# Optimization experiments

Hardware: AMD Instinct MI355X
Metric: run time of the kernel (lower is better)

The kernel has to match this reference:

```python
import jax, jax.numpy as jnp
import numpy as np
from itertools import product

B = 2
X, Y, Z = 96, 96, 192          # voxel grid (x, y, t)
NPB = 300_000                   # occupied voxels per batch item
PX, PY, PZ = X // 2, Y // 2, Z // 4  # pooled grid (kernel/stride [2,2,4])
CIN, COUT, KVOL, NCONV = 32, 64, 27, 2
EPS = 1e-5


def _build_maps():
    """Builds sparse coordinates, maxpool segment ids and 3x3x3 conv kernel maps
    (gather/scatter index pairs per kernel offset), mirroring MinkowskiEngine's
    coordinate manager."""
    rng = np.random.default_rng(0)
    coords = []
    for b in range(B):
        lin = rng.choice(X * Y * Z, NPB, replace=False)
        x = lin // (Y * Z)
        y = (lin // Z) % Y
        z = lin % Z
        coords.append(np.stack([np.full(NPB, b), x, y, z], 1))
    c = np.concatenate(coords).astype(np.int64)  # [N,4] (b,x,y,z)
    # max-pool coord map: out coord = (x//2, y//2, z//4)
    pk = ((c[:, 0] * PX + c[:, 1] // 2) * PY + c[:, 2] // 2) * PZ + c[:, 3] // 4
    uniq, inv = np.unique(pk, return_inverse=True)
    M = len(uniq)
    pz = uniq % PZ
    py = (uniq // PZ) % PY
    px = (uniq // (PZ * PY)) % PX
    pb = uniq // (PZ * PY * PX)
    lut = np.full(B * PX * PY * PZ, -1, np.int64)
    lut[uniq] = np.arange(M)
    ins, outs = [], []
    for dx, dy, dz in product((-1, 0, 1), repeat=3):
        nx, ny, nz = px + dx, py + dy, pz + dz
        ok = (nx >= 0) & (nx < PX) & (ny >= 0) & (ny < PY) & (nz >= 0) & (nz < PZ)
        nk = ((pb * PX + np.clip(nx, 0, PX - 1)) * PY + np.clip(ny, 0, PY - 1)) * PZ + np.clip(nz, 0, PZ - 1)
        j = np.where(ok, lut[nk], -1)
        sel = j >= 0
        ins.append(j[sel])
        outs.append(np.arange(M)[sel])
    L = max(len(a) for a in ins)
    ci = np.full((KVOL, L), M, np.int64)  # pad -> index M (zero row)
    co = np.full((KVOL, L), M, np.int64)  # pad -> dummy out row M (dropped)
    for k in range(KVOL):
        ci[k, : len(ins[k])] = ins[k]
        co[k, : len(outs[k])] = outs[k]
    return inv.astype(np.int64), ci, co, M


def setup_inputs() -> dict:
    key = jax.random.key(0)
    ks = jax.random.split(key, 4)
    pool_seg, ci, co, M = _build_maps()
    N = B * NPB
    feats = jax.random.normal(ks[0], (N, CIN), jnp.float32)
    Wd = jax.random.normal(ks[1], (CIN, COUT), jnp.float32) / np.sqrt(CIN)
    W1 = jax.random.normal(ks[2], (KVOL, COUT, COUT), jnp.float32) / np.sqrt(KVOL * COUT)
    W2 = jax.random.normal(ks[3], (KVOL, COUT, COUT), jnp.float32) / np.sqrt(KVOL * COUT)
    ones = jnp.ones((COUT,), jnp.float32)
    zeros = jnp.zeros((COUT,), jnp.float32)
    return {
        "feats": feats, "Wd": Wd,
        "g0": ones, "b0": zeros,
        "W1": W1, "g1": ones, "b1": zeros,
        "W2": W2, "g2": ones, "b2": zeros,
        "pool_seg": jnp.asarray(pool_seg),
        "conv_in": jnp.asarray(ci), "conv_out": jnp.asarray(co),
        "num_pooled": int(M),
    }


def _bn(h, g, b):
    # training-mode batch norm over all sparse points (biased variance, eps=1e-5)
    m = h.mean(0)
    v = jnp.mean((h - m) ** 2, 0)
    return (h - m) * (g / jnp.sqrt(v + EPS)) + b


def _sparse_conv(h, W, conv_in, conv_out, M):
    # gather-GEMM-scatter over 27 kernel offsets (MinkowskiConvolution, bias=False)
    C = W.shape[-1]
    hp = jnp.concatenate([h, jnp.zeros((1, h.shape[1]), h.dtype)])  # zero pad row
    out = jnp.zeros((M + 1, C), h.dtype)
    for k in range(W.shape[0]):
        out = out.at[conv_out[k]].add(hp[conv_in[k]] @ W[k])
    return out[:M]


def reference(feats, Wd, g0, b0, W1, g1, b1, W2, g2, b2,
              pool_seg, conv_in, conv_out, num_pooled):
    # down_conv (1x1, bias=False) -> BN -> ELU
    h = jax.nn.elu(_bn(feats @ Wd, g0, b0))
    # MinkowskiMaxPooling kernel=stride=[2,2,4] == segment max over pooled cells
    down = jax.ops.segment_max(h, pool_seg, num_segments=num_pooled)
    # nConvs LUConv blocks: ELU(BN(conv3x3x3(x)))
    o = down
    for W, g, b in ((W1, g1, b1), (W2, g2, b2)):
        o = jax.nn.elu(_bn(_sparse_conv(o, W, conv_in, conv_out, num_pooled), g, b))
    # residual add + ELU
    return jax.nn.elu(o + down)
```

## Files before the change

### kernel.cpp

```cpp
#include <hip/hip_runtime.h>
#include <math.h>

#define CIN  32
#define COUT 64
#define KVOL 27
#define EPSF 1e-5f

typedef __attribute__((ext_vector_type(8))) short          short8;
typedef __attribute__((ext_vector_type(8))) unsigned short u16x8;
typedef __attribute__((ext_vector_type(4))) float          float4v;

__device__ __forceinline__ float eluf(float x) { return x > 0.f ? x : expm1f(x); }

__device__ __forceinline__ unsigned short f2bf(float x) {
    unsigned u = __float_as_uint(x);
    unsigned r = (u + 0x7FFFu + ((u >> 16) & 1u)) >> 16;
    return (unsigned short)r;
}
__device__ __forceinline__ unsigned pk2bf(float lo, float hi) {
    return (unsigned)f2bf(lo) | ((unsigned)f2bf(hi) << 16);
}
__device__ __forceinline__ float bf2f(unsigned short h) {
    return __uint_as_float(((unsigned)h) << 16);
}

__global__ void cvt_w_kernel(const float* __restrict__ W1, const float* __restrict__ W2,
                             const float* __restrict__ Wd,
                             unsigned short* __restrict__ Wt1, unsigned short* __restrict__ Wt2,
                             unsigned short* __restrict__ Wdt)
{
    int b = blockIdx.x;
    int t = threadIdx.x;
    if (b == 54) {
        for (int e = t; e < CIN * COUT; e += 256) {
            int i = e >> 6, c = e & 63;
            Wdt[c * CIN + i] = f2bf(Wd[e]);
        }
        return;
    }
    const float* W = (b < 27) ? W1 : W2;
    unsigned short* Wt = (b < 27) ? Wt1 : Wt2;
    int k = (b < 27) ? b : b - 27;
    const float* src = W + (size_t)k * (COUT * COUT);
    unsigned short* dst = Wt + (size_t)k * (COUT * COUT);
    for (int e = t; e < COUT * COUT; e += 256) {
        int i = e >> 6, c = e & 63;
        dst[c * COUT + i] = f2bf(src[e]);
    }
}

__global__ __launch_bounds__(256) void gemm_t_kernel(
    const float* __restrict__ feats, const unsigned short* __restrict__ Wdt,
    int N, unsigned short* __restrict__ t_bf, float* __restrict__ red0)
{
    __shared__ float red_s[64];
    __shared__ float red_q[64];
    int t = threadIdx.x;
    if (t < 64) { red_s[t] = 0.f; red_q[t] = 0.f; }
    __syncthreads();

    int w = t >> 6, lane = t & 63, l15 = lane & 15, quad = lane >> 4;

    short8 aw[4];
    #pragma unroll
    for (int mt = 0; mt < 4; ++mt)
        aw[mt] = *(const short8*)(Wdt + (size_t)(16 * mt + l15) * CIN + quad * 8);

    float s1[16], sq[16];
    #pragma unroll
    for (int e = 0; e < 16; ++e) { s1[e] = 0.f; sq[e] = 0.f; }

    int numTiles = (N + 15) >> 4;
    int stride = gridDim.x * 4;
    int tile = blockIdx.x * 4 + w;

    float4 c0 = make_float4(0.f, 0.f, 0.f, 0.f), c1 = c0;
    {
        int pt = tile * 16 + l15;
        if (tile < numTiles && pt < N) {
            const float4* s = (const float4*)(feats + (size_t)pt * CIN + quad * 8);
            c0 = s[0]; c1 = s[1];
        }
    }

    while (tile < numTiles) {
        int nt = tile + stride;
        float4 n0 = make_float4(0.f, 0.f, 0.f, 0.f), n1 = n0;
        {
            int npt = nt * 16 + l15;
            if (nt < numTiles && npt < N) {
                const float4* s = (const float4*)(feats + (size_t)npt * CIN + quad * 8);
                n0 = s[0]; n1 = s[1];
            }
        }
        union { short8 v; unsigned u[4]; } b;
        b.u[0] = pk2bf(c0.x, c0.y);
        b.u[1] = pk2bf(c0.z, c0.w);
        b.u[2] = pk2bf(c1.x, c1.y);
        b.u[3] = pk2bf(c1.z, c1.w);

        float4v acc[4];
        #pragma unroll
        for (int mt = 0; mt < 4; ++mt)
            acc[mt] = __builtin_amdgcn_mfma_f32_16x16x32_bf16(
                aw[mt], b.v, (float4v){0.f, 0.f, 0.f, 0.f}, 0, 0, 0);

        int pt = tile * 16 + l15;
        if (pt < N) {
            #pragma unroll
            for (int mt = 0; mt < 4; ++mt) {
                uint2 o;
                o.x = pk2bf(acc[mt][0], acc[mt][1]);
                o.y = pk2bf(acc[mt][2], acc[mt][3]);
                *(uint2*)(t_bf + (size_t)pt * COUT + mt * 16 + quad * 4) = o;
            }
        }
        #pragma unroll
        for (int mt = 0; mt < 4; ++mt)
            #pragma unroll
            for (int e = 0; e < 4; ++e) {
                float v = acc[mt][e];
                s1[mt * 4 + e] += v; sq[mt * 4 + e] += v * v;
            }
        c0 = n0; c1 = n1;
        tile = nt;
    }

    #pragma unroll
    for (int m = 1; m <= 8; m <<= 1) {
        #pragma unroll
        for (int e = 0; e < 16; ++e) {
            s1[e] += __shfl_xor(s1[e], m);
            sq[e] += __shfl_xor(sq[e], m);
        }
    }
    if (l15 == 0) {
        #pragma unroll
        for (int e = 0; e < 16; ++e) {
            int ch = (e >> 2) * 16 + quad * 4 + (e & 3);
            atomicAdd(&red_s[ch], s1[e]);
            atomicAdd(&red_q[ch], sq[e]);
        }
    }
    __syncthreads();
    float* dst = red0 + (size_t)(blockIdx.x & 3) * 128;
    if (t < 64)       atomicAdd(&dst[t], red_s[t]);
    else if (t < 128) atomicAdd(&dst[t], red_q[t - 64]);
}

__global__ void fin0_kernel(const float* __restrict__ red, const float* __restrict__ g,
                            const float* __restrict__ b, float* __restrict__ scale,
                            float* __restrict__ shift, int cnt)
{
    int c = threadIdx.x;
    float s = 0.f, q = 0.f;
    #pragma unroll
    for (int i = 0; i < 4; ++i) { s += red[i * 128 + c]; q += red[i * 128 + 64 + c]; }
    float m = s / (float)cnt;
    float var = q / (float)cnt - m * m;
    float sc = g[c] / sqrtf(var + EPSF);
    scale[c] = sc;
    shift[c] = b[c] - m * sc;
}

__global__ void bucket_kernel(const int* __restrict__ pool_seg,
                              int* __restrict__ cnt, int* __restrict__ bucket, int N)
{
    int j = blockIdx.x * 256 + threadIdx.x;
    if (j < N) {
        int s = pool_seg[j];
        int pos = atomicAdd(&cnt[s], 1);
        bucket[(size_t)s * 16 + pos] = j;
    }
}

__global__ __launch_bounds__(256) void pool_max_kernel(
    const unsigned short* __restrict__ t_bf,
    const int* __restrict__ cnt, const int* __restrict__ bucket,
    const float* __restrict__ scale0, const float* __restrict__ shift0,
    unsigned short* __restrict__ down_bf, int M)
{
    int id = blockIdx.x * 256 + threadIdx.x;
    int s = id >> 4, cg = id & 15;
    if (s >= M) return;
    int n = cnt[s];
    const int4* bk4 = (const int4*)(bucket + (size_t)s * 16);
    float4 mx = make_float4(-INFINITY, -INFINITY, -INFINITY, -INFINITY);
    float4 mn = make_float4( INFINITY,  INFINITY,  INFINITY,  INFINITY);
    #pragma unroll
    for (int ch = 0; ch < 4; ++ch) {
        if (ch * 4 >= n) break;
        int4 b4 = bk4[ch];
        #pragma unroll
        for (int e = 0; e < 4; ++e) {
            int p = ch * 4 + e;
            if (p < n) {
                int idx = (e == 0) ? b4.x : (e == 1) ? b4.y : (e == 2) ? b4.z : b4.w;
                ushort4 v = *(const ushort4*)(t_bf + (size_t)idx * COUT + cg * 4);
                float f0 = bf2f(v.x), f1 = bf2f(v.y), f2 = bf2f(v.z), f3 = bf2f(v.w);
                mx.x = fmaxf(mx.x, f0); mn.x = fminf(mn.x, f0);
                mx.y = fmaxf(mx.y, f1); mn.y = fminf(mn.y, f1);
                mx.z = fmaxf(mx.z, f2); mn.z = fminf(mn.z, f2);
                mx.w = fmaxf(mx.w, f3); mn.w = fminf(mn.w, f3);
            }
        }
    }
    int c0 = cg * 4;
    float4 sc = *(const float4*)(scale0 + c0);
    float4 sh = *(const float4*)(shift0 + c0);
    ushort4 o;
    o.x = f2bf(eluf(sc.x * (sc.x >= 0.f ? mx.x : mn.x) + sh.x));
    o.y = f2bf(eluf(sc.y * (sc.y >= 0.f ? mx.y : mn.y) + sh.y));
    o.z = f2bf(eluf(sc.z * (sc.z >= 0.f ? mx.z : mn.z) + sh.z));
    o.w = f2bf(eluf(sc.w * (sc.w >= 0.f ? mx.w : mn.w) + sh.w));
    *(ushort4*)(down_bf + (size_t)s * COUT + c0) = o;
}

__global__ void nbr_kernel(const int* __restrict__ conv_out, const int* __restrict__ conv_in,
                           int* __restrict__ nbrT, int L, int M)
{
    int k = blockIdx.y;
    int idx = blockIdx.x * 256 + threadIdx.x;
    if (idx < L) {
        int e = k * L + idx;
        int j = conv_out[e];
        if (j < M) nbrT[(size_t)k * M + j] = conv_in[e];
    }
}

__global__ void bn_elu_cvt_kernel(const float* __restrict__ o1,
                                  const float* __restrict__ scale,
                                  const float* __restrict__ shift,
                                  unsigned short* __restrict__ o1t, int n)
{
    int i = blockIdx.x * 256 + threadIdx.x;
    if (i < n) {
        int c = i & 63;
        o1t[i] = f2bf(eluf(o1[i] * scale[c] + shift[c]));
    }
}

__global__ __launch_bounds__(256) void conv_mfma_kernel(
    const unsigned short* __restrict__ in, const unsigned short* __restrict__ Wt,
    const int* __restrict__ nbrT, int M,
    float* __restrict__ out, float* __restrict__ red)
{
    __shared__ __align__(16) unsigned short A_lds[128 * 72];
    __shared__ __align__(16) unsigned short W_lds[64 * 72];
    __shared__ float red_s[64];
    __shared__ float red_q[64];
    int t = threadIdx.x;
    int base = blockIdx.x * 128;
    int w = t >> 6, lane = t & 63, l15 = lane & 15, quad = lane >> 4;

    if (t < 64) { red_s[t] = 0.f; red_q[t] = 0.f; }

    float4v acc[2][4];
    #pragma unroll
    for (int s = 0; s < 2; ++s)
        #pragma unroll
        for (int n = 0; n < 4; ++n)
            acc[s][n] = (float4v){0.f, 0.f, 0.f, 0.f};

    int ar = t >> 1, ah = t & 1;
    int gj = base + ar;
    int wc = t >> 2, wq = t & 3;

    for (int k = 0; k < KVOL; ++k) {
        __syncthreads();
        {
            int idx = (gj < M) ? nbrT[(size_t)k * M + gj] : -1;
            u16x8 c0 = {0,0,0,0,0,0,0,0}, c1 = c0, c2 = c0, c3 = c0;
            if (idx >= 0) {
                const u16x8* src = (const u16x8*)(in + (size_t)idx * COUT + 32 * ah);
                c0 = src[0]; c1 = src[1]; c2 = src[2]; c3 = src[3];
            }
            u16x8* dst = (u16x8*)(A_lds + ar * 72 + 32 * ah);
            dst[0] = c0; dst[1] = c1; dst[2] = c2; dst[3] = c3;
        }
        {
            const u16x8* src = (const u16x8*)(Wt + (size_t)k * (COUT * COUT) + wc * COUT + 16 * wq);
            u16x8* dst = (u16x8*)(W_lds + wc * 72 + 16 * wq);
            dst[0] = src[0]; dst[1] = src[1];
        }
        __syncthreads();
        #pragma unroll
        for (int kk = 0; kk < 64; kk += 32) {
            short8 a0 = *(const short8*)(A_lds + (32 * w + l15) * 72 + kk + quad * 8);
            short8 a1 = *(const short8*)(A_lds + (32 * w + 16 + l15) * 72 + kk + quad * 8);
            #pragma unroll
            for (int n = 0; n < 4; ++n) {
                short8 b = *(const short8*)(W_lds + (16 * n + l15) * 72 + kk + quad * 8);
                acc[0][n] = __builtin_amdgcn_mfma_f32_16x16x32_bf16(a0, b, acc[0][n], 0, 0, 0);
                acc[1][n] = __builtin_amdgcn_mfma_f32_16x16x32_bf16(a1, b, acc[1][n], 0, 0, 0);
            }
        }
    }

    #pragma unroll
    for (int s = 0; s < 2; ++s) {
        int row = base + 32 * w + 16 * s + quad * 4;
        #pragma unroll
        for (int n = 0; n < 4; ++n) {
            int c = 16 * n + l15;
            #pragma unroll
            for (int e = 0; e < 4; ++e)
                if (row + e < M) out[(size_t)(row + e) * COUT + c] = acc[s][n][e];
        }
    }
    #pragma unroll
    for (int n = 0; n < 4; ++n) {
        float s1 = 0.f, sq = 0.f;
        #pragma unroll
        for (int s = 0; s < 2; ++s)
            #pragma unroll
            for (int e = 0; e < 4; ++e) { float v = acc[s][n][e]; s1 += v; sq += v * v; }
        s1 += __shfl_xor(s1, 16); sq += __shfl_xor(sq, 16);
        s1 += __shfl_xor(s1, 32); sq += __shfl_xor(sq, 32);
        if (quad == 0) {
            atomicAdd(&red_s[16 * n + l15], s1);
            atomicAdd(&red_q[16 * n + l15], sq);
        }
    }
    __syncthreads();
    if (t < 64)       atomicAdd(&red[t], red_s[t]);
    else if (t < 128) atomicAdd(&red[t], red_q[t - 64]);
}

__global__ void finC_kernel(const float* __restrict__ red, const float* __restrict__ g,
                            const float* __restrict__ b, float* __restrict__ scale,
                            float* __restrict__ shift, int M)
{
    int c = threadIdx.x;
    float m = red[c] / (float)M;
    float var = red[64 + c] / (float)M - m * m;
    float sc = g[c] / sqrtf(var + EPSF);
    scale[c] = sc;
    shift[c] = b[c] - m * sc;
}

__global__ void final_kernel(float* __restrict__ out, const unsigned short* __restrict__ down_bf,
                             const float* __restrict__ scale2, const float* __restrict__ shift2,
                             int n)
{
    int i = blockIdx.x * 256 + threadIdx.x;
    if (i < n) {
        int c = i & 63;
        float y = eluf(out[i] * scale2[c] + shift2[c]);
        out[i] = eluf(y + bf2f(down_bf[i]));
    }
}

extern "C" void kernel_launch(void* const* d_in, const int* in_sizes, int n_in,
                              void* d_out, int out_size, void* d_ws, size_t ws_size,
                              hipStream_t stream)
{
    (void)n_in; (void)ws_size;
    const float* feats    = (const float*)d_in[0];
    const float* Wd       = (const float*)d_in[1];
    const float* g0       = (const float*)d_in[2];
    const float* b0       = (const float*)d_in[3];
    const float* W1       = (const float*)d_in[4];
    const float* g1       = (const float*)d_in[5];
    const float* b1       = (const float*)d_in[6];
    const float* W2       = (const float*)d_in[7];
    const float* g2       = (const float*)d_in[8];
    const float* b2       = (const float*)d_in[9];
    const int*   pool_seg = (const int*)d_in[10];
    const int*   conv_in  = (const int*)d_in[11];
    const int*   conv_out = (const int*)d_in[12];

    int N = in_sizes[0] / CIN;
    int M = out_size / COUT;
    int L = in_sizes[11] / KVOL;

    char* ws = (char*)d_ws;
    size_t off = 0;
    auto alloc = [&](size_t bytes) -> void* {
        void* p = ws + off;
        off = (off + bytes + 255) & ~(size_t)255;
        return p;
    };
    float*          o1      = (float*)alloc((size_t)M * COUT * 4);
    unsigned short* down_bf = (unsigned short*)alloc((size_t)M * COUT * 2);
    unsigned short* o1t     = (unsigned short*)alloc((size_t)M * COUT * 2);
    unsigned short* t_bf    = (unsigned short*)alloc((size_t)N * COUT * 2);
    int*            nbrT    = (int*)alloc((size_t)KVOL * M * 4);
    unsigned short* Wt1     = (unsigned short*)alloc((size_t)KVOL * COUT * COUT * 2);
    unsigned short* Wt2     = (unsigned short*)alloc((size_t)KVOL * COUT * COUT * 2);
    unsigned short* Wdt     = (unsigned short*)alloc((size_t)CIN * COUT * 2);
    int*            cnt     = (int*)alloc((size_t)M * 4);
    int*            bucket  = (int*)alloc((size_t)M * 16 * 4);
    float* red  = (float*)alloc((size_t)768 * 4);
    float* red0 = red, *red1 = red + 512, *red2 = red + 640;
    float* sreg = (float*)alloc((size_t)6 * 64 * 4);
    float* scale0 = sreg, *shift0 = sreg + 64;
    float* scale1 = sreg + 128, *shift1 = sreg + 192;
    float* scale2 = sreg + 256, *shift2 = sreg + 320;

    hipMemsetAsync(nbrT, 0xFF, (size_t)KVOL * M * 4, stream);
    hipMemsetAsync(cnt, 0, (size_t)M * 4, stream);
    hipMemsetAsync(red, 0, (size_t)768 * 4, stream);

    cvt_w_kernel<<<55, 256, 0, stream>>>(W1, W2, Wd, Wt1, Wt2, Wdt);
    gemm_t_kernel<<<1024, 256, 0, stream>>>(feats, Wdt, N, t_bf, red0);
    fin0_kernel<<<1, 64, 0, stream>>>(red0, g0, b0, scale0, shift0, N);
    bucket_kernel<<<(N + 255) / 256, 256, 0, stream>>>(pool_seg, cnt, bucket, N);
    pool_max_kernel<<<(M * 16 + 255) / 256, 256, 0, stream>>>(
        t_bf, cnt, bucket, scale0, shift0, down_bf, M);
    dim3 gn((L + 255) / 256, KVOL);
    nbr_kernel<<<gn, 256, 0, stream>>>(conv_out, conv_in, nbrT, L, M);

    int cblocks = (M + 127) / 128;
    conv_mfma_kernel<<<cblocks, 256, 0, stream>>>(down_bf, Wt1, nbrT, M, o1, red1);
    finC_kernel<<<1, 64, 0, stream>>>(red1, g1, b1, scale1, shift1, M);
    bn_elu_cvt_kernel<<<(M * COUT + 255) / 256, 256, 0, stream>>>(o1, scale1, shift1, o1t, M * COUT);
    conv_mfma_kernel<<<cblocks, 256, 0, stream>>>(o1t, Wt2, nbrT, M, (float*)d_out, red2);
    finC_kernel<<<1, 64, 0, stream>>>(red2, g2, b2, scale2, shift2, M);
    final_kernel<<<(M * COUT + 255) / 256, 256, 0, stream>>>(
        (float*)d_out, down_bf, scale2, shift2, M * COUT);
}
```

Baseline: 549.9 us.

## Double-buffer conv gather with XOR-swizzled LDS and vectorize elementwise kernels

The sparse conv kernel now keeps two LDS buffers and an XOR swizzle instead of padding. It loads the next kernel offset's gathered rows and weights into registers while the MFMAs run on the current buffer, which drops one barrier per iteration. The BN+ELU conversion kernel and the final residual kernel are changed to process four elements per thread with vector loads. The cost is twice the LDS, more registers for the prefetched data, and a possible drop in occupancy.

```diff
diff --git a/kernel.cpp b/kernel.cpp
--- a/kernel.cpp
+++ b/kernel.cpp
@@ -231,12 +231,20 @@
 __global__ void bn_elu_cvt_kernel(const float* __restrict__ o1,
                                   const float* __restrict__ scale,
                                   const float* __restrict__ shift,
-                                  unsigned short* __restrict__ o1t, int n)
+                                  unsigned short* __restrict__ o1t, int n4)
 {
     int i = blockIdx.x * 256 + threadIdx.x;
-    if (i < n) {
-        int c = i & 63;
-        o1t[i] = f2bf(eluf(o1[i] * scale[c] + shift[c]));
+    if (i < n4) {
+        float4 v = ((const float4*)o1)[i];
+        int c0 = (i & 15) * 4;
+        float4 sc = *(const float4*)(scale + c0);
+        float4 sh = *(const float4*)(shift + c0);
+        ushort4 o;
+        o.x = f2bf(eluf(v.x * sc.x + sh.x));
+        o.y = f2bf(eluf(v.y * sc.y + sh.y));
+        o.z = f2bf(eluf(v.z * sc.z + sh.z));
+        o.w = f2bf(eluf(v.w * sc.w + sh.w));
+        ((ushort4*)o1t)[i] = o;
     }
 }
 
@@ -245,8 +253,8 @@
     const int* __restrict__ nbrT, int M,
     float* __restrict__ out, float* __restrict__ red)
 {
-    __shared__ __align__(16) unsigned short A_lds[128 * 72];
-    __shared__ __align__(16) unsigned short W_lds[64 * 72];
+    __shared__ __align__(16) unsigned short A_lds[2][128 * 64];
+    __shared__ __align__(16) unsigned short W_lds[2][64 * 64];
     __shared__ float red_s[64];
     __shared__ float red_q[64];
     int t = threadIdx.x;
@@ -265,36 +273,79 @@
     int ar = t >> 1, ah = t & 1;
     int gj = base + ar;
     int wc = t >> 2, wq = t & 3;
+    int arx = ar & 7;
+    int wcx = wc & 7;
+
+    const u16x8 z8 = (u16x8){0, 0, 0, 0, 0, 0, 0, 0};
+
+    {
+        int idx0 = (gj < M) ? nbrT[gj] : -1;
+        u16x8 a0 = z8, a1 = z8, a2 = z8, a3 = z8;
+        if (idx0 >= 0) {
+            const u16x8* src = (const u16x8*)(in + (size_t)idx0 * COUT);
+            a0 = src[ah * 4 + 0]; a1 = src[ah * 4 + 1];
+            a2 = src[ah * 4 + 2]; a3 = src[ah * 4 + 3];
+        }
+        const u16x8* ws = (const u16x8*)(Wt + (size_t)wc * COUT);
+        u16x8 w0 = ws[wq * 2], w1 = ws[wq * 2 + 1];
+
+        unsigned short* Ab = A_lds[0];
+        *(u16x8*)(Ab + ar * 64 + ((ah * 4 + 0) ^ arx) * 8) = a0;
+        *(u16x8*)(Ab + ar * 64 + ((ah * 4 + 1) ^ arx) * 8) = a1;
+        *(u16x8*)(Ab + ar * 64 + ((ah * 4 + 2) ^ arx) * 8) = a2;
+        *(u16x8*)(Ab + ar * 64 + ((ah * 4 + 3) ^ arx) * 8) = a3;
+        unsigned short* Wb = W_lds[0];
+        *(u16x8*)(Wb + wc * 64 + ((wq * 2 + 0) ^ wcx) * 8) = w0;
+        *(u16x8*)(Wb + wc * 64 + ((wq * 2 + 1) ^ wcx) * 8) = w1;
+    }
+    int idxN = (gj < M) ? nbrT[(size_t)M + gj] : -1;
+    __syncthreads();
 
     for (int k = 0; k < KVOL; ++k) {
-        __syncthreads();
-        {
-            int idx = (gj < M) ? nbrT[(size_t)k * M + gj] : -1;
-            u16x8 c0 = {0,0,0,0,0,0,0,0}, c1 = c0, c2 = c0, c3 = c0;
-            if (idx >= 0) {
-                const u16x8* src = (const u16x8*)(in + (size_t)idx * COUT + 32 * ah);
-                c0 = src[0]; c1 = src[1]; c2 = src[2]; c3 = src[3];
-            }
-            u16x8* dst = (u16x8*)(A_lds + ar * 72 + 32 * ah);
-            dst[0] = c0; dst[1] = c1; dst[2] = c2; dst[3] = c3;
-        }
-        {
-            const u16x8* src = (const u16x8*)(Wt + (size_t)k * (COUT * COUT) + wc * COUT + 16 * wq);
-            u16x8* dst = (u16x8*)(W_lds + wc * 72 + 16 * wq);
-            dst[0] = src[0]; dst[1] = src[1];
-        }
-        __syncthreads();
+        int cur = k & 1;
+        bool pf = (k + 1 < KVOL);
+
+        u16x8 na0 = z8, na1 = z8, na2 = z8, na3 = z8, nw0 = z8, nw1 = z8;
+        if (pf) {
+            if (idxN >= 0) {
+                const u16x8* src = (const u16x8*)(in + (size_t)idxN * COUT);
+                na0 = src[ah * 4 + 0]; na1 = src[ah * 4 + 1];
+                na2 = src[ah * 4 + 2]; na3 = src[ah * 4 + 3];
+            }
+            const u16x8* ws = (const u16x8*)(Wt + (size_t)(k + 1) * (COUT * COUT) + (size_t)wc * COUT);
+            nw0 = ws[wq * 2]; nw1 = ws[wq * 2 + 1];
+            idxN = (k + 2 < KVOL && gj < M) ? nbrT[(size_t)(k + 2) * M + gj] : -1;
+        }
+
+        const unsigned short* Ab = A_lds[cur];
+        const unsigned short* Wb = W_lds[cur];
         #pragma unroll
         for (int kk = 0; kk < 64; kk += 32) {
-            short8 a0 = *(const short8*)(A_lds + (32 * w + l15) * 72 + kk + quad * 8);
-            short8 a1 = *(const short8*)(A_lds + (32 * w + 16 + l15) * 72 + kk + quad * 8);
+            int slb = quad + (kk >> 3);
+            int r0 = 32 * w + l15;
+            short8 a0 = *(const short8*)(Ab + r0 * 64 + ((slb ^ (r0 & 7)) * 8));
+            int r1 = r0 + 16;
+            short8 a1 = *(const short8*)(Ab + r1 * 64 + ((slb ^ (r1 & 7)) * 8));
             #pragma unroll
             for (int n = 0; n < 4; ++n) {
-                short8 b = *(const short8*)(W_lds + (16 * n + l15) * 72 + kk + quad * 8);
+                int rb = 16 * n + l15;
+                short8 b = *(const short8*)(Wb + rb * 64 + ((slb ^ (rb & 7)) * 8));
                 acc[0][n] = __builtin_amdgcn_mfma_f32_16x16x32_bf16(a0, b, acc[0][n], 0, 0, 0);
                 acc[1][n] = __builtin_amdgcn_mfma_f32_16x16x32_bf16(a1, b, acc[1][n], 0, 0, 0);
             }
         }
+
+        if (pf) {
+            unsigned short* An = A_lds[cur ^ 1];
+            *(u16x8*)(An + ar * 64 + ((ah * 4 + 0) ^ arx) * 8) = na0;
+            *(u16x8*)(An + ar * 64 + ((ah * 4 + 1) ^ arx) * 8) = na1;
+            *(u16x8*)(An + ar * 64 + ((ah * 4 + 2) ^ arx) * 8) = na2;
+            *(u16x8*)(An + ar * 64 + ((ah * 4 + 3) ^ arx) * 8) = na3;
+            unsigned short* Wn = W_lds[cur ^ 1];
+            *(u16x8*)(Wn + wc * 64 + ((wq * 2 + 0) ^ wcx) * 8) = nw0;
+            *(u16x8*)(Wn + wc * 64 + ((wq * 2 + 1) ^ wcx) * 8) = nw1;
+        }
+        __syncthreads();
     }
 
     #pragma unroll
@@ -341,13 +392,20 @@
 
 __global__ void final_kernel(float* __restrict__ out, const unsigned short* __restrict__ down_bf,
                              const float* __restrict__ scale2, const float* __restrict__ shift2,
-                             int n)
+                             int n4)
 {
     int i = blockIdx.x * 256 + threadIdx.x;
-    if (i < n) {
-        int c = i & 63;
-        float y = eluf(out[i] * scale2[c] + shift2[c]);
-        out[i] = eluf(y + bf2f(down_bf[i]));
+    if (i < n4) {
+        float4 v = ((const float4*)out)[i];
+        ushort4 d = ((const ushort4*)down_bf)[i];
+        int c0 = (i & 15) * 4;
+        float4 sc = *(const float4*)(scale2 + c0);
+        float4 sh = *(const float4*)(shift2 + c0);
+        v.x = eluf(eluf(v.x * sc.x + sh.x) + bf2f(d.x));
+        v.y = eluf(eluf(v.y * sc.y + sh.y) + bf2f(d.y));
+        v.z = eluf(eluf(v.z * sc.z + sh.z) + bf2f(d.z));
+        v.w = eluf(eluf(v.w * sc.w + sh.w) + bf2f(d.w));
+        ((float4*)out)[i] = v;
     }
 }
 
@@ -414,9 +472,10 @@
     int cblocks = (M + 127) / 128;
     conv_mfma_kernel<<<cblocks, 256, 0, stream>>>(down_bf, Wt1, nbrT, M, o1, red1);
     finC_kernel<<<1, 64, 0, stream>>>(red1, g1, b1, scale1, shift1, M);
-    bn_elu_cvt_kernel<<<(M * COUT + 255) / 256, 256, 0, stream>>>(o1, scale1, shift1, o1t, M * COUT);
+    int n4 = (M * COUT) / 4;
+    bn_elu_cvt_kernel<<<(n4 + 255) / 256, 256, 0, stream>>>(o1, scale1, shift1, o1t, n4);
     conv_mfma_kernel<<<cblocks, 256, 0, stream>>>(o1t, Wt2, nbrT, M, (float*)d_out, red2);
     finC_kernel<<<1, 64, 0, stream>>>(red2, g2, b2, scale2, shift2, M);
-    final_kernel<<<(M * COUT + 255) / 256, 256, 0, stream>>>(
-        (float*)d_out, down_bf, scale2, shift2, M * COUT);
-}
+    final_kernel<<<(n4 + 255) / 256, 256, 0, stream>>>(
+        (float*)d_out, down_bf, scale2, shift2, n4);
+}
```

Measured after the change: 529.4 us. -3.7%, faster.
